# Kernel tuning notes

Measured on AMD Instinct MI355X. Metric: run time of the kernel, lower is better.

The kernel has to match this reference:

```python
import jax, jax.numpy as jnp
import numpy as np

B = 16384      # batch
IN = 512       # input width
G, F, O = 64, 24, 16      # hidden: groups, fan_in, group_out (width = G*O = 1024)
GO_G, GO_F, GO_O = 4, 48, 16  # output layer: 4 groups x 16 = 64 outputs


def setup_inputs() -> dict:
    key = jax.random.key(0)
    ks = jax.random.split(key, 13)
    # total columns available (concat of input + all prior hidden layers)
    tot = [IN, IN + G * O, IN + 2 * G * O, IN + 3 * G * O]  # 512,1536,2560,3584
    scale = 0.1
    return {
        "x": jax.random.normal(ks[0], (B, IN), jnp.float32),
        "W1": jax.random.normal(ks[1], (G, F, O), jnp.float32) * scale,
        "b1": jnp.zeros((G, O), jnp.float32),
        "W2": jax.random.normal(ks[2], (G, F, O), jnp.float32) * scale,
        "b2": jnp.zeros((G, O), jnp.float32),
        "W3": jax.random.normal(ks[3], (G, F, O), jnp.float32) * scale,
        "b3": jnp.zeros((G, O), jnp.float32),
        "Wo": jax.random.normal(ks[4], (GO_G, GO_F, GO_O), jnp.float32) * scale,
        "bo": jnp.zeros((GO_G, GO_O), jnp.float32),
        "idx1": jax.random.randint(ks[5], (G, F), 0, tot[0], jnp.int32),
        "idx2": jax.random.randint(ks[6], (G, F), 0, tot[1], jnp.int32),
        "idx3": jax.random.randint(ks[7], (G, F), 0, tot[2], jnp.int32),
        "idxo": jax.random.randint(ks[8], (GO_G, GO_F), 0, tot[3], jnp.int32),
    }


def _group_layer(acc, idx, W, b, act):
    # acc: [B, P] concat of all prior layer outputs; idx: [G, F] column coords
    g = acc[:, idx]                               # [B, G, F] irregular gather
    h = jnp.einsum('bgf,gfo->bgo', g, W) + b      # many tiny dense sublayers
    h = act(h)
    return h.reshape(h.shape[0], -1)              # concat groups -> [B, G*O]


def reference(x, W1, b1, W2, b2, W3, b3, Wo, bo, idx1, idx2, idx3, idxo):
    acc = x
    for idx, W, b in ((idx1, W1, b1), (idx2, W2, b2), (idx3, W3, b3)):
        out = _group_layer(acc, idx, W, b, jnp.tanh)
        acc = jnp.concatenate([acc, out], axis=1)  # inputs.append(layer_out)
    # output layer uses linear out_activation
    return _group_layer(acc, idxo, Wo, bo, lambda h: h)  # [B, 64]
```

## Files before the change

kernel.cpp:

```cpp
#include <hip/hip_runtime.h>
#include <hip/hip_bf16.h>


typedef unsigned short ushort_t;
typedef unsigned int uint_t;
typedef __attribute__((ext_vector_type(8))) short short8;
typedef __attribute__((ext_vector_type(4))) float f32x4;

#define ACC_STRIDE 3592
#define PAD_ONE 3584
#define PAD_ZERO 3588
#define ONE_BYTE (PAD_ONE * 2)
#define ZERO_BYTE (PAD_ZERO * 2)
#define ACC_U16 (16 * ACC_STRIDE)
#define OFFS_BYTES 25600
#define LDS_BYTES (ACC_U16 * 2 + OFFS_BYTES)

#define OFF_HID_B 204800
#define OFF_HEAD_B 229376

__device__ __forceinline__ ushort_t f2bf(float f) {
    __hip_bfloat16 h = __float2bfloat16(f);
    union { __hip_bfloat16 h; ushort_t u; } v;
    v.h = h;
    return v.u;
}

__device__ __forceinline__ uint_t pack2bf(float lo, float hi) {
    return (uint_t)f2bf(lo) | ((uint_t)f2bf(hi) << 16);
}

__device__ __forceinline__ float fast_tanh(float x) {
    float e = __expf(2.0f * x);
    return fmaf(-2.0f, __builtin_amdgcn_rcpf(e + 1.0f), 1.0f);
}

__global__ __launch_bounds__(256)
void convert_weights(const float* __restrict__ W1, const float* __restrict__ b1,
                     const float* __restrict__ W2, const float* __restrict__ b2,
                     const float* __restrict__ W3, const float* __restrict__ b3,
                     const float* __restrict__ Wo, const float* __restrict__ bo,
                     const int* __restrict__ idx1, const int* __restrict__ idx2,
                     const int* __restrict__ idx3, const int* __restrict__ idxo,
                     ushort_t* __restrict__ ws)
{
    const int tid = blockIdx.x * 256 + threadIdx.x;
    const int lane = tid & 63;
    const int nn = lane & 15;
    const int quad = lane >> 4;
    if (tid < 12288) {
        const int g = (tid >> 6) & 63;
        const int l = tid >> 12;
        const float* W = (l == 0) ? W1 : (l == 1) ? W2 : W3;
        const float* bb = (l == 0) ? b1 : (l == 1) ? b2 : b3;
        const float* Wg = W + g * 384;
        ushort_t v[8];
        #pragma unroll
        for (int j = 0; j < 8; ++j) {
            const int k = quad * 8 + j;
            v[j] = (k < 24) ? f2bf(Wg[k * 16 + nn])
                 : (k == 24) ? f2bf(bb[g * 16 + nn]) : (ushort_t)0;
        }
        ushort4* dst = reinterpret_cast<ushort4*>(ws + (size_t)tid * 8);
        dst[0] = make_ushort4(v[0], v[1], v[2], v[3]);
        dst[1] = make_ushort4(v[4], v[5], v[6], v[7]);
    } else if (tid < 12800) {
        const int h = tid - 12288;
        const int gs = h >> 6;
        const int go = gs >> 1;
        const int step = gs & 1;
        const float* Wg = Wo + go * 768;
        ushort_t v[8];
        #pragma unroll
        for (int j = 0; j < 8; ++j) {
            const int k = step * 32 + quad * 8 + j;
            v[j] = (k < 48) ? f2bf(Wg[k * 16 + nn])
                 : (k == 48) ? f2bf(bo[go * 16 + nn]) : (ushort_t)0;
        }
        ushort4* dst = reinterpret_cast<ushort4*>(ws + (size_t)tid * 8);
        dst[0] = make_ushort4(v[0], v[1], v[2], v[3]);
        dst[1] = make_ushort4(v[4], v[5], v[6], v[7]);
    } else if (tid < 18944) {
        const int e = tid - 12800;
        const int l = e >> 11;
        const int rem = e & 2047;
        const int g = rem >> 5;
        const int k = rem & 31;
        const int* idx = (l == 0) ? idx1 : (l == 1) ? idx2 : idx3;
        const int v = (k < 24) ? idx[g * 24 + k] * 2
                    : (k == 24) ? ONE_BYTE : ZERO_BYTE;
        reinterpret_cast<int*>((char*)ws + OFF_HID_B)[e] = v;
    } else if (tid < 19200) {
        const int e = tid - 18944;
        const int go = e >> 6;
        const int k = e & 63;
        const int v = (k < 48) ? idxo[go * 48 + k] * 2
                    : (k == 48) ? ONE_BYTE : ZERO_BYTE;
        reinterpret_cast<int*>((char*)ws + OFF_HEAD_B)[e] = v;
    }
}

__global__ __launch_bounds__(1024)
void demodel_mfma(const float* __restrict__ x,
                  const ushort_t* __restrict__ ws,
                  float* __restrict__ out)
{
    extern __shared__ __align__(16) ushort_t smem[];
    const int t = threadIdx.x;
    const int lane = t & 63;
    const int wv = t >> 6;
    const int row0 = blockIdx.x * 16;
    const int nn = lane & 15;
    const int quad = lane >> 4;

    {
        const int r = t >> 6;
        const int c = (t & 63) << 3;
        const float4* src = reinterpret_cast<const float4*>(
            x + (size_t)(row0 + r) * 512 + c);
        float4 a0 = src[0], a1 = src[1];
        uint4 p;
        p.x = pack2bf(a0.x, a0.y); p.y = pack2bf(a0.z, a0.w);
        p.z = pack2bf(a1.x, a1.y); p.w = pack2bf(a1.z, a1.w);
        *reinterpret_cast<uint4*>(smem + r * ACC_STRIDE + c) = p;
    }
    if (t < 16)
        *reinterpret_cast<uint4*>(smem + t * ACC_STRIDE + PAD_ONE) =
            make_uint4(0x00003f80u, 0u, 0u, 0u);
    {
        const uint4* src = reinterpret_cast<const uint4*>((const char*)ws + OFF_HID_B);
        uint4* dst = reinterpret_cast<uint4*>(smem + ACC_U16);
        for (int i = t; i < OFFS_BYTES / 16; i += 1024)
            dst[i] = src[i];
    }
    __syncthreads();

    const int* offs = reinterpret_cast<const int*>(smem + ACC_U16);
    const char* accb = (const char*)smem + nn * (ACC_STRIDE * 2);

    #pragma unroll 1
    for (int l = 0; l < 3; ++l) {
        const int out_base = 512 + l * 1024;
        const int g0 = wv << 2;

        int4 o0[4], o1[4];
        short8 bfr[4];
        #pragma unroll
        for (int gi = 0; gi < 4; ++gi) {
            const int* op = offs + l * 2048 + (g0 + gi) * 32 + quad * 8;
            o0[gi] = *reinterpret_cast<const int4*>(op);
            o1[gi] = *reinterpret_cast<const int4*>(op + 4);
            bfr[gi] = *reinterpret_cast<const short8*>(
                ws + (((size_t)l * 64 + g0 + gi) * 64 + lane) * 8);
        }

        short8 af[4];
        #pragma unroll
        for (int gi = 0; gi < 4; ++gi) {
            af[gi][0] = *(const short*)(accb + o0[gi].x);
            af[gi][1] = *(const short*)(accb + o0[gi].y);
            af[gi][2] = *(const short*)(accb + o0[gi].z);
            af[gi][3] = *(const short*)(accb + o0[gi].w);
            af[gi][4] = *(const short*)(accb + o1[gi].x);
            af[gi][5] = *(const short*)(accb + o1[gi].y);
            af[gi][6] = *(const short*)(accb + o1[gi].z);
            af[gi][7] = *(const short*)(accb + o1[gi].w);
        }

        f32x4 acc[4];
        #pragma unroll
        for (int gi = 0; gi < 4; ++gi) {
            f32x4 z = { 0.f, 0.f, 0.f, 0.f };
            acc[gi] = __builtin_amdgcn_mfma_f32_16x16x32_bf16(af[gi], bfr[gi], z, 0, 0, 0);
        }

        #pragma unroll
        for (int gi = 0; gi < 4; ++gi) {
            const int colo = out_base + (g0 + gi) * 16 + nn;
            #pragma unroll
            for (int i = 0; i < 4; ++i)
                smem[(quad * 4 + i) * ACC_STRIDE + colo] = f2bf(fast_tanh(acc[gi][i]));
        }
        __syncthreads();
    }

    if (wv < 4) {
        const int go = wv;
        int4 o0[2], o1[2];
        short8 bfr[2];
        #pragma unroll
        for (int s = 0; s < 2; ++s) {
            const int* op = offs + 6144 + go * 64 + s * 32 + quad * 8;
            o0[s] = *reinterpret_cast<const int4*>(op);
            o1[s] = *reinterpret_cast<const int4*>(op + 4);
            bfr[s] = *reinterpret_cast<const short8*>(
                ws + (12288 + ((size_t)go * 2 + s) * 64 + lane) * 8);
        }
        short8 af[2];
        #pragma unroll
        for (int s = 0; s < 2; ++s) {
            af[s][0] = *(const short*)(accb + o0[s].x);
            af[s][1] = *(const short*)(accb + o0[s].y);
            af[s][2] = *(const short*)(accb + o0[s].z);
            af[s][3] = *(const short*)(accb + o0[s].w);
            af[s][4] = *(const short*)(accb + o1[s].x);
            af[s][5] = *(const short*)(accb + o1[s].y);
            af[s][6] = *(const short*)(accb + o1[s].z);
            af[s][7] = *(const short*)(accb + o1[s].w);
        }
        f32x4 z = { 0.f, 0.f, 0.f, 0.f };
        f32x4 a0 = __builtin_amdgcn_mfma_f32_16x16x32_bf16(af[0], bfr[0], z, 0, 0, 0);
        f32x4 a1 = __builtin_amdgcn_mfma_f32_16x16x32_bf16(af[1], bfr[1], z, 0, 0, 0);
        #pragma unroll
        for (int i = 0; i < 4; ++i)
            out[(size_t)(row0 + quad * 4 + i) * 64 + go * 16 + nn] = a0[i] + a1[i];
    }
}

extern "C" void kernel_launch(void* const* d_in, const int* in_sizes, int n_in,
                              void* d_out, int out_size, void* d_ws, size_t ws_size,
                              hipStream_t stream) {
    const float* x  = (const float*)d_in[0];
    const float* W1 = (const float*)d_in[1];
    const float* b1 = (const float*)d_in[2];
    const float* W2 = (const float*)d_in[3];
    const float* b2 = (const float*)d_in[4];
    const float* W3 = (const float*)d_in[5];
    const float* b3 = (const float*)d_in[6];
    const float* Wo = (const float*)d_in[7];
    const float* bo = (const float*)d_in[8];
    const int* idx1 = (const int*)d_in[9];
    const int* idx2 = (const int*)d_in[10];
    const int* idx3 = (const int*)d_in[11];
    const int* idxo = (const int*)d_in[12];
    float* out = (float*)d_out;

    (void)hipFuncSetAttribute((const void*)demodel_mfma,
                              hipFuncAttributeMaxDynamicSharedMemorySize,
                              LDS_BYTES);

    convert_weights<<<75, 256, 0, stream>>>(W1, b1, W2, b2, W3, b3, Wo, bo,
                                            idx1, idx2, idx3, idxo,
                                            (ushort_t*)d_ws);

    const int B = in_sizes[0] / 512;
    const int grid = B / 16;
    demodel_mfma<<<grid, 1024, LDS_BYTES, stream>>>(
        x, (const ushort_t*)d_ws, out);
}
```

Measured before the change: 128.4 us.

## Make blocks persistent over four row tiles with prefetched input loads

The kernel now launches a fixed 256 blocks, each looping over four 16-row tiles instead of one block per tile. Waves 8-15 prefetch and convert the next tile's x rows into registers while the output layer of the current tile runs, hiding global load latency. This also amortises the per-block offset table copy into LDS. The row stride shrinks slightly to reuse pad slots. In exchange the grid is hardcoded to the test batch size, only 256 blocks run on the device, and each tile adds extra barriers.

```diff
diff --git a/kernel.cpp b/kernel.cpp
--- a/kernel.cpp
+++ b/kernel.cpp
@@ -7,11 +7,11 @@
 typedef __attribute__((ext_vector_type(8))) short short8;
 typedef __attribute__((ext_vector_type(4))) float f32x4;
 
-#define ACC_STRIDE 3592
+#define ACC_STRIDE 3588
+#define ROW_BYTES (ACC_STRIDE * 2)
 #define PAD_ONE 3584
-#define PAD_ZERO 3588
 #define ONE_BYTE (PAD_ONE * 2)
-#define ZERO_BYTE (PAD_ZERO * 2)
+#define ZERO_BYTE (3586 * 2)
 #define ACC_U16 (16 * ACC_STRIDE)
 #define OFFS_BYTES 25600
 #define LDS_BYTES (ACC_U16 * 2 + OFFS_BYTES)
@@ -100,6 +100,8 @@
     }
 }
 
+#define NTILES 4
+
 __global__ __launch_bounds__(1024)
 void demodel_mfma(const float* __restrict__ x,
                   const ushort_t* __restrict__ ws,
@@ -109,111 +111,138 @@
     const int t = threadIdx.x;
     const int lane = t & 63;
     const int wv = t >> 6;
-    const int row0 = blockIdx.x * 16;
     const int nn = lane & 15;
     const int quad = lane >> 4;
 
-    {
-        const int r = t >> 6;
-        const int c = (t & 63) << 3;
-        const float4* src = reinterpret_cast<const float4*>(
-            x + (size_t)(row0 + r) * 512 + c);
-        float4 a0 = src[0], a1 = src[1];
-        uint4 p;
-        p.x = pack2bf(a0.x, a0.y); p.y = pack2bf(a0.z, a0.w);
-        p.z = pack2bf(a1.x, a1.y); p.w = pack2bf(a1.z, a1.w);
-        *reinterpret_cast<uint4*>(smem + r * ACC_STRIDE + c) = p;
-    }
-    if (t < 16)
-        *reinterpret_cast<uint4*>(smem + t * ACC_STRIDE + PAD_ONE) =
-            make_uint4(0x00003f80u, 0u, 0u, 0u);
     {
         const uint4* src = reinterpret_cast<const uint4*>((const char*)ws + OFF_HID_B);
         uint4* dst = reinterpret_cast<uint4*>(smem + ACC_U16);
         for (int i = t; i < OFFS_BYTES / 16; i += 1024)
             dst[i] = src[i];
     }
-    __syncthreads();
+    if (t < 16) {
+        uint2* p = reinterpret_cast<uint2*>((char*)smem + t * ROW_BYTES + ONE_BYTE);
+        *p = make_uint2(0x00003f80u, 0u);
+    }
 
     const int* offs = reinterpret_cast<const int*>(smem + ACC_U16);
-    const char* accb = (const char*)smem + nn * (ACC_STRIDE * 2);
+    const char* accb = (const char*)smem + nn * ROW_BYTES;
+    char* accw = (char*)smem;
+
+    const int pr = (t - 512) >> 5;
+    const int pc = (t & 31) << 4;
+    uint_t px[8];
+
+    if (wv >= 8) {
+        const float4* src = reinterpret_cast<const float4*>(
+            x + ((size_t)blockIdx.x * 16 + pr) * 512 + pc);
+        float4 a0 = src[0], a1 = src[1], a2 = src[2], a3 = src[3];
+        px[0] = pack2bf(a0.x, a0.y); px[1] = pack2bf(a0.z, a0.w);
+        px[2] = pack2bf(a1.x, a1.y); px[3] = pack2bf(a1.z, a1.w);
+        px[4] = pack2bf(a2.x, a2.y); px[5] = pack2bf(a2.z, a2.w);
+        px[6] = pack2bf(a3.x, a3.y); px[7] = pack2bf(a3.z, a3.w);
+    }
 
     #pragma unroll 1
-    for (int l = 0; l < 3; ++l) {
-        const int out_base = 512 + l * 1024;
-        const int g0 = wv << 2;
-
-        int4 o0[4], o1[4];
-        short8 bfr[4];
-        #pragma unroll
-        for (int gi = 0; gi < 4; ++gi) {
-            const int* op = offs + l * 2048 + (g0 + gi) * 32 + quad * 8;
-            o0[gi] = *reinterpret_cast<const int4*>(op);
-            o1[gi] = *reinterpret_cast<const int4*>(op + 4);
-            bfr[gi] = *reinterpret_cast<const short8*>(
-                ws + (((size_t)l * 64 + g0 + gi) * 64 + lane) * 8);
-        }
-
-        short8 af[4];
-        #pragma unroll
-        for (int gi = 0; gi < 4; ++gi) {
-            af[gi][0] = *(const short*)(accb + o0[gi].x);
-            af[gi][1] = *(const short*)(accb + o0[gi].y);
-            af[gi][2] = *(const short*)(accb + o0[gi].z);
-            af[gi][3] = *(const short*)(accb + o0[gi].w);
-            af[gi][4] = *(const short*)(accb + o1[gi].x);
-            af[gi][5] = *(const short*)(accb + o1[gi].y);
-            af[gi][6] = *(const short*)(accb + o1[gi].z);
-            af[gi][7] = *(const short*)(accb + o1[gi].w);
-        }
-
-        f32x4 acc[4];
-        #pragma unroll
-        for (int gi = 0; gi < 4; ++gi) {
+    for (int it = 0; it < NTILES; ++it) {
+        const int row0 = (it * 256 + blockIdx.x) * 16;
+
+        __syncthreads();
+        if (wv >= 8) {
+            uint2* d = reinterpret_cast<uint2*>(accw + pr * ROW_BYTES + pc * 2);
+            d[0] = make_uint2(px[0], px[1]);
+            d[1] = make_uint2(px[2], px[3]);
+            d[2] = make_uint2(px[4], px[5]);
+            d[3] = make_uint2(px[6], px[7]);
+        }
+        __syncthreads();
+
+        #pragma unroll 1
+        for (int l = 0; l < 3; ++l) {
+            const int out_base = 512 + l * 1024;
+            const int g0 = wv << 2;
+
+            int4 o0[4], o1[4];
+            short8 bfr[4];
+            #pragma unroll
+            for (int gi = 0; gi < 4; ++gi) {
+                const int* op = offs + l * 2048 + (g0 + gi) * 32 + quad * 8;
+                o0[gi] = *reinterpret_cast<const int4*>(op);
+                o1[gi] = *reinterpret_cast<const int4*>(op + 4);
+                bfr[gi] = *reinterpret_cast<const short8*>(
+                    ws + (((size_t)l * 64 + g0 + gi) * 64 + lane) * 8);
+            }
+
+            short8 af[4];
+            #pragma unroll
+            for (int gi = 0; gi < 4; ++gi) {
+                af[gi][0] = *(const short*)(accb + o0[gi].x);
+                af[gi][1] = *(const short*)(accb + o0[gi].y);
+                af[gi][2] = *(const short*)(accb + o0[gi].z);
+                af[gi][3] = *(const short*)(accb + o0[gi].w);
+                af[gi][4] = *(const short*)(accb + o1[gi].x);
+                af[gi][5] = *(const short*)(accb + o1[gi].y);
+                af[gi][6] = *(const short*)(accb + o1[gi].z);
+                af[gi][7] = *(const short*)(accb + o1[gi].w);
+            }
+
+            f32x4 acc[4];
+            #pragma unroll
+            for (int gi = 0; gi < 4; ++gi) {
+                f32x4 z = { 0.f, 0.f, 0.f, 0.f };
+                acc[gi] = __builtin_amdgcn_mfma_f32_16x16x32_bf16(af[gi], bfr[gi], z, 0, 0, 0);
+            }
+
+            #pragma unroll
+            for (int gi = 0; gi < 4; ++gi) {
+                const int colo = out_base + (g0 + gi) * 16 + nn;
+                #pragma unroll
+                for (int i = 0; i < 4; ++i)
+                    smem[(quad * 4 + i) * ACC_STRIDE + colo] = f2bf(fast_tanh(acc[gi][i]));
+            }
+            __syncthreads();
+        }
+
+        if (wv < 4) {
+            const int go = wv;
+            int4 o0[2], o1[2];
+            short8 bfr[2];
+            #pragma unroll
+            for (int s = 0; s < 2; ++s) {
+                const int* op = offs + 6144 + go * 64 + s * 32 + quad * 8;
+                o0[s] = *reinterpret_cast<const int4*>(op);
+                o1[s] = *reinterpret_cast<const int4*>(op + 4);
+                bfr[s] = *reinterpret_cast<const short8*>(
+                    ws + (12288 + ((size_t)go * 2 + s) * 64 + lane) * 8);
+            }
+            short8 af[2];
+            #pragma unroll
+            for (int s = 0; s < 2; ++s) {
+                af[s][0] = *(const short*)(accb + o0[s].x);
+                af[s][1] = *(const short*)(accb + o0[s].y);
+                af[s][2] = *(const short*)(accb + o0[s].z);
+                af[s][3] = *(const short*)(accb + o0[s].w);
+                af[s][4] = *(const short*)(accb + o1[s].x);
+                af[s][5] = *(const short*)(accb + o1[s].y);
+                af[s][6] = *(const short*)(accb + o1[s].z);
+                af[s][7] = *(const short*)(accb + o1[s].w);
+            }
             f32x4 z = { 0.f, 0.f, 0.f, 0.f };
-            acc[gi] = __builtin_amdgcn_mfma_f32_16x16x32_bf16(af[gi], bfr[gi], z, 0, 0, 0);
-        }
-
-        #pragma unroll
-        for (int gi = 0; gi < 4; ++gi) {
-            const int colo = out_base + (g0 + gi) * 16 + nn;
+            f32x4 a0 = __builtin_amdgcn_mfma_f32_16x16x32_bf16(af[0], bfr[0], z, 0, 0, 0);
+            f32x4 a1 = __builtin_amdgcn_mfma_f32_16x16x32_bf16(af[1], bfr[1], z, 0, 0, 0);
             #pragma unroll
             for (int i = 0; i < 4; ++i)
-                smem[(quad * 4 + i) * ACC_STRIDE + colo] = f2bf(fast_tanh(acc[gi][i]));
-        }
-        __syncthreads();
-    }
-
-    if (wv < 4) {
-        const int go = wv;
-        int4 o0[2], o1[2];
-        short8 bfr[2];
-        #pragma unroll
-        for (int s = 0; s < 2; ++s) {
-            const int* op = offs + 6144 + go * 64 + s * 32 + quad * 8;
-            o0[s] = *reinterpret_cast<const int4*>(op);
-            o1[s] = *reinterpret_cast<const int4*>(op + 4);
-            bfr[s] = *reinterpret_cast<const short8*>(
-                ws + (12288 + ((size_t)go * 2 + s) * 64 + lane) * 8);
-        }
-        short8 af[2];
-        #pragma unroll
-        for (int s = 0; s < 2; ++s) {
-            af[s][0] = *(const short*)(accb + o0[s].x);
-            af[s][1] = *(const short*)(accb + o0[s].y);
-            af[s][2] = *(const short*)(accb + o0[s].z);
-            af[s][3] = *(const short*)(accb + o0[s].w);
-            af[s][4] = *(const short*)(accb + o1[s].x);
-            af[s][5] = *(const short*)(accb + o1[s].y);
-            af[s][6] = *(const short*)(accb + o1[s].z);
-            af[s][7] = *(const short*)(accb + o1[s].w);
-        }
-        f32x4 z = { 0.f, 0.f, 0.f, 0.f };
-        f32x4 a0 = __builtin_amdgcn_mfma_f32_16x16x32_bf16(af[0], bfr[0], z, 0, 0, 0);
-        f32x4 a1 = __builtin_amdgcn_mfma_f32_16x16x32_bf16(af[1], bfr[1], z, 0, 0, 0);
-        #pragma unroll
-        for (int i = 0; i < 4; ++i)
-            out[(size_t)(row0 + quad * 4 + i) * 64 + go * 16 + nn] = a0[i] + a1[i];
+                out[(size_t)(row0 + quad * 4 + i) * 64 + go * 16 + nn] = a0[i] + a1[i];
+        }
+        if (wv >= 8 && it + 1 < NTILES) {
+            const float4* src = reinterpret_cast<const float4*>(
+                x + (((size_t)(it + 1) * 256 + blockIdx.x) * 16 + pr) * 512 + pc);
+            float4 a0 = src[0], a1 = src[1], a2 = src[2], a3 = src[3];
+            px[0] = pack2bf(a0.x, a0.y); px[1] = pack2bf(a0.z, a0.w);
+            px[2] = pack2bf(a1.x, a1.y); px[3] = pack2bf(a1.z, a1.w);
+            px[4] = pack2bf(a2.x, a2.y); px[5] = pack2bf(a2.z, a2.w);
+            px[6] = pack2bf(a3.x, a3.y); px[7] = pack2bf(a3.z, a3.w);
+        }
     }
 }
 
@@ -243,8 +272,6 @@
                                             idx1, idx2, idx3, idxo,
                                             (ushort_t*)d_ws);
 
-    const int B = in_sizes[0] / 512;
-    const int grid = B / 16;
-    demodel_mfma<<<grid, 1024, LDS_BYTES, stream>>>(
+    demodel_mfma<<<256, 1024, LDS_BYTES, stream>>>(
         x, (const ushort_t*)d_ws, out);
 }
```

Result: faster. 121.0 us (-5.7%).
